# Performance work log

Hardware: AMD Instinct MI355X
Metric: run time of the kernel (lower is better)

## Reference

```python
import jax, jax.numpy as jnp
import numpy as np
import math

D_MODEL = 1024
NUM_HEADS = 16
HEAD_DIM = D_MODEL // NUM_HEADS
REPETITIONS = 3
NEG = -10000.0


def setup_inputs() -> dict:
    key = jax.random.key(0)
    ks = jax.random.split(key, 5)
    B, S = 2, 2048
    x = jax.random.normal(ks[0], (B, S, D_MODEL), dtype=jnp.float32)
    Wqkv_w = jax.random.normal(ks[1], (3 * D_MODEL, D_MODEL), dtype=jnp.float32) * (1.0 / math.sqrt(D_MODEL))
    Wqkv_b = jax.random.normal(ks[2], (3 * D_MODEL,), dtype=jnp.float32) * 0.02
    out_w = jax.random.normal(ks[3], (D_MODEL, D_MODEL), dtype=jnp.float32) * (1.0 / math.sqrt(D_MODEL))
    out_b = jax.random.normal(ks[4], (D_MODEL,), dtype=jnp.float32) * 0.02
    return {"x": x, "Wqkv_w": Wqkv_w, "Wqkv_b": Wqkv_b, "out_w": out_w, "out_b": out_b}


def _self_attention(q, k, v, mask):
    # q,k,v: (B,S,H,D); mask: (S,S) additive causal (-10000 above diagonal)
    scale = 1.0 / math.sqrt(q.shape[-1])
    scores = jnp.einsum('bthd,bshd->bhts', q, k * scale) + mask  # (B,H,S,S)
    attn = jax.nn.softmax(scores, axis=-1)
    return jnp.einsum('bhts,bshd->bthd', attn, v)  # (B,S,H,D)


def reference(x, Wqkv_w, Wqkv_b, out_w, out_b):
    B, S, _ = x.shape
    qkv = x @ Wqkv_w.T + Wqkv_b                       # (B,S,3*D_MODEL)
    qkv = qkv.reshape(B, S, 3, NUM_HEADS, HEAD_DIM)
    q, k, v = qkv[:, :, 0], qkv[:, :, 1], qkv[:, :, 2]
    mask = jnp.triu(jnp.full((S, S), NEG, dtype=x.dtype), 1)
    context = _self_attention(q, k, v, mask)
    # recurrent re-attention: rep_dim == 'q' -> query replaced by previous context
    for _ in range(REPETITIONS - 1):
        context = _self_attention(context, k, v, mask)
    out = context.reshape(B, S, D_MODEL) @ out_w.T + out_b
    return out
```

## Files before the change

### kernel.cpp

```cpp
#include <hip/hip_runtime.h>


#define D_MODEL 1024
#define NHEADS  16
#define HD      64
#define SEQ     2048
#define BATCH   2
#define NROWS   (BATCH*SEQ)
#define NQKV    (3*D_MODEL)
#define SCL2F   0.1803368801111601f
#define MASK2   (-14426.950408889634f)

typedef __bf16 bf16x8 __attribute__((ext_vector_type(8)));
typedef float  f32x4  __attribute__((ext_vector_type(4)));
typedef unsigned short us8 __attribute__((ext_vector_type(8)));
typedef unsigned short us4 __attribute__((ext_vector_type(4)));
typedef short  s16x4  __attribute__((ext_vector_type(4)));

__device__ __forceinline__ unsigned short f2bf(float f) {
  unsigned int u = __float_as_uint(f);
  u = (u + 0x7fffu + ((u >> 16) & 1u)) >> 16;
  return (unsigned short)u;
}

union Pack8 { us8 v; unsigned short e[8]; };
union Pack4 { us4 v; unsigned short e[4]; };

__device__ __forceinline__ us8 cvt8(const float4 &a, const float4 &b) {
  Pack8 p;
  p.e[0]=f2bf(a.x); p.e[1]=f2bf(a.y); p.e[2]=f2bf(a.z); p.e[3]=f2bf(a.w);
  p.e[4]=f2bf(b.x); p.e[5]=f2bf(b.y); p.e[6]=f2bf(b.z); p.e[7]=f2bf(b.w);
  return p.v;
}

__device__ __forceinline__ void gl_lds16(const unsigned short* g, unsigned short* l) {
  __builtin_amdgcn_global_load_lds(
      (const __attribute__((address_space(1))) unsigned int*)g,
      (__attribute__((address_space(3))) unsigned int*)l, 16, 0, 0);
}

#define CVT_N1 (NROWS*D_MODEL)
#define CVT_N2 (NQKV*D_MODEL)
#define CVT_N3 (D_MODEL*D_MODEL)

__global__ __launch_bounds__(256) void cvt_all(
    const float* __restrict__ x, const float* __restrict__ wq,
    const float* __restrict__ ow,
    unsigned short* __restrict__ xb, unsigned short* __restrict__ wqb,
    unsigned short* __restrict__ owb)
{
  size_t i = ((size_t)blockIdx.x * 256 + threadIdx.x) * 8;
  const float* src; unsigned short* dst; size_t off;
  if (i < CVT_N1)                { src = x;  dst = xb;  off = i; }
  else if (i < CVT_N1 + CVT_N2)  { src = wq; dst = wqb; off = i - CVT_N1; }
  else                           { src = ow; dst = owb; off = i - CVT_N1 - CVT_N2; }
  float4 a = *(const float4*)(src + off);
  float4 b = *(const float4*)(src + off + 4);
  *(us8*)(dst + off) = cvt8(a, b);
}

__global__ __launch_bounds__(256) void qkv_gemm(
    const unsigned short* __restrict__ xb, const unsigned short* __restrict__ wqb,
    const float* __restrict__ bias,
    unsigned short* __restrict__ q, unsigned short* __restrict__ k,
    unsigned short* __restrict__ vT)
{
  __shared__ __align__(16) unsigned short As[128*64];
  __shared__ __align__(16) unsigned short Bs[128*64];
  const int tid = threadIdx.x;
  const int m0 = blockIdx.y * 128, n0 = blockIdx.x * 128;
  const int wave = tid >> 6, lane = tid & 63;
  const int wm = (wave >> 1) * 64, wn = (wave & 1) * 64;
  const int lrow = lane & 15, quad = lane >> 4;

  const int dr = lane >> 3;
  const int pg = lane & 7;
  const int sg = (pg ^ dr) * 8;
  const unsigned short* gA[4]; const unsigned short* gB[4];
  unsigned short *lA[4], *lB[4];
  #pragma unroll
  for (int i = 0; i < 4; i++) {
    int c = wave*4 + i;
    gA[i] = xb  + (size_t)(m0 + c*8 + dr) * D_MODEL + sg;
    gB[i] = wqb + (size_t)(n0 + c*8 + dr) * D_MODEL + sg;
    lA[i] = &As[c*512];
    lB[i] = &Bs[c*512];
  }
  const int px0 = (quad ^ (lrow & 7)) * 8;
  const int px1 = ((quad + 4) ^ (lrow & 7)) * 8;

  f32x4 acc[4][4];
  #pragma unroll
  for (int i = 0; i < 4; i++)
    #pragma unroll
    for (int j = 0; j < 4; j++) acc[i][j] = (f32x4){0.f,0.f,0.f,0.f};

  for (int k0 = 0; k0 < D_MODEL; k0 += 64) {
    __syncthreads();
    #pragma unroll
    for (int i = 0; i < 4; i++) { gl_lds16(gA[i] + k0, lA[i]); gl_lds16(gB[i] + k0, lB[i]); }
    __syncthreads();
    bf16x8 af[4][2], bfr[4][2];
    #pragma unroll
    for (int mf = 0; mf < 4; mf++) {
      int row = wm + mf*16 + lrow;
      af[mf][0] = *(const bf16x8*)&As[row*64 + px0];
      af[mf][1] = *(const bf16x8*)&As[row*64 + px1];
    }
    #pragma unroll
    for (int nb = 0; nb < 4; nb++) {
      int row = wn + nb*16 + lrow;
      bfr[nb][0] = *(const bf16x8*)&Bs[row*64 + px0];
      bfr[nb][1] = *(const bf16x8*)&Bs[row*64 + px1];
    }
    #pragma unroll
    for (int h = 0; h < 2; h++)
      #pragma unroll
      for (int mf = 0; mf < 4; mf++)
        #pragma unroll
        for (int nb = 0; nb < 4; nb++)
          acc[mf][nb] = __builtin_amdgcn_mfma_f32_16x16x32_bf16(af[mf][h], bfr[nb][h], acc[mf][nb], 0, 0, 0);
  }

  #pragma unroll
  for (int mf = 0; mf < 4; mf++) {
    #pragma unroll
    for (int nb = 0; nb < 4; nb++) {
      int n = n0 + wn + nb*16 + lrow;
      int which = n >> 10;
      int h  = (n >> 6) & 15;
      int hd = n & 63;
      int mb = m0 + wm + mf*16 + quad*4;
      int b  = mb >> 11;
      int s  = mb & 2047;
      float bi = bias[n];
      if (which == 2) {
        Pack4 p4;
        #pragma unroll
        for (int r = 0; r < 4; r++) p4.e[r] = f2bf(acc[mf][nb][r] + bi);
        *(us4*)&vT[((size_t)((b*NHEADS + h)*HD + hd))*SEQ + s] = p4.v;
      } else {
        unsigned short* dst = (which == 0) ? q : k;
        float scl = (which == 0) ? SCL2F : 1.0f;
        #pragma unroll
        for (int r = 0; r < 4; r++)
          dst[(size_t)((b*NHEADS + h)*SEQ + s + r)*HD + hd] = f2bf((acc[mf][nb][r] + bi) * scl);
      }
    }
  }
}

#define LDQ 72

__global__ __launch_bounds__(512, 4) void attn3(
    const unsigned short* __restrict__ qg,
    const unsigned short* __restrict__ kg,
    const unsigned short* __restrict__ vTg,
    unsigned short* __restrict__ ctx)
{
  __shared__ __align__(16) unsigned short Ks[4][64*LDQ];
  __shared__ __align__(16) unsigned short Vs[4][64*LDQ];
  unsigned short* QC = &Vs[0][0];

  const int tid  = threadIdx.x;
  const int w    = tid >> 6, lane = tid & 63;
  const int lrow = lane & 15, quad = lane >> 4;
  const int bh = blockIdx.x;
  const int yy = blockIdx.y;
  const int base = (blockIdx.x + yy) & 7;
  const int qt = (yy < 8) ? base : (15 - base);
  const unsigned short* qbase = qg  + (size_t)bh * SEQ * HD;
  const unsigned short* kbase = kg  + (size_t)bh * SEQ * HD;
  const unsigned short* vbase = vTg + (size_t)bh * HD * SEQ;
  unsigned short* cbase = ctx + (size_t)bh * SEQ * HD;

  const int srow = tid >> 3;
  const int sco  = (tid & 7) * 8;
  const int qrow = tid >> 2, qc0 = (tid & 3) * 16;
  const bool vsw = (w & 1);
  const int vq = (quad*4) ^ ((lrow >> 3) << 2);

  {
    const unsigned short* src = qbase + (size_t)(qt*128 + qrow)*HD + qc0;
    *(uint4*)&QC[qrow*LDQ + qc0]     = *(const uint4*)src;
    *(uint4*)&QC[qrow*LDQ + qc0 + 8] = *(const uint4*)(src + 8);
  }
  __syncthreads();

  bf16x8 qb0 = *(const bf16x8*)&QC[(w*16 + lrow)*LDQ + quad*8];
  bf16x8 qb1 = *(const bf16x8*)&QC[(w*16 + lrow)*LDQ + 32 + quad*8];
  __syncthreads();

  const int qwbase = qt*128 + w*16;
  const int npair = qt + 1;

  for (int rep = 0; rep < 3; ++rep) {
    f32x4 od[4];
    #pragma unroll
    for (int df = 0; df < 4; df++) od[df] = (f32x4){0.f,0.f,0.f,0.f};
    float ls = 0.f;

    uint4 ka, kb, va, vb;
    {
      const unsigned short* ks = kbase + (size_t)srow*HD + sco;
      ka = *(const uint4*)ks;  kb = *(const uint4*)(ks + 64*HD);
      const unsigned short* vs = vbase + (size_t)srow*SEQ + sco;
      va = *(const uint4*)vs;  vb = *(const uint4*)(vs + 64);
    }

    for (int t = 0; t < npair; ++t) {
      const int pb = (t & 1) * 2;
      *(uint4*)&Ks[pb][srow*LDQ + sco]   = ka;
      *(uint4*)&Ks[pb+1][srow*LDQ + sco] = kb;
      {
        uint4 vaS = vsw ? make_uint4(va.z, va.w, va.x, va.y) : va;
        uint4 vbS = vsw ? make_uint4(vb.z, vb.w, vb.x, vb.y) : vb;
        *(uint4*)&Vs[pb][srow*LDQ + sco]   = vaS;
        *(uint4*)&Vs[pb+1][srow*LDQ + sco] = vbS;
      }
      if (t + 1 < npair) {
        const unsigned short* ks = kbase + (size_t)((2*t+2)*64 + srow)*HD + sco;
        ka = *(const uint4*)ks;  kb = *(const uint4*)(ks + 64*HD);
        const unsigned short* vs = vbase + (size_t)srow*SEQ + (2*t+2)*64 + sco;
        va = *(const uint4*)vs;  vb = *(const uint4*)(vs + 64);
      }
      __syncthreads();

      #pragma unroll
      for (int half = 0; half < 2; ++half) {
        const int bb = pb + half;
        const int sbase = (2*t + half) * 64;
        if (sbase > qwbase + 15) continue;
        f32x4 sc[4];
        __builtin_amdgcn_s_setprio(1);
        #pragma unroll
        for (int sf = 0; sf < 4; sf++) {
          bf16x8 a0 = *(const bf16x8*)&Ks[bb][(sf*16 + lrow)*LDQ + quad*8];
          bf16x8 a1 = *(const bf16x8*)&Ks[bb][(sf*16 + lrow)*LDQ + 32 + quad*8];
          f32x4 z = (f32x4){0.f,0.f,0.f,0.f};
          z = __builtin_amdgcn_mfma_f32_16x16x32_bf16(a0, qb0, z, 0, 0, 0);
          z = __builtin_amdgcn_mfma_f32_16x16x32_bf16(a1, qb1, z, 0, 0, 0);
          sc[sf] = z;
        }
        __builtin_amdgcn_s_setprio(0);
        if (sbase + 63 > qwbase) {
          int ql = qwbase + lrow;
          #pragma unroll
          for (int sf = 0; sf < 4; sf++)
            #pragma unroll
            for (int r = 0; r < 4; r++)
              if (sbase + sf*16 + quad*4 + r > ql) sc[sf][r] += MASK2;
        }
        s16x4 pf[4];
        float lp = 0.f;
        #pragma unroll
        for (int sf = 0; sf < 4; sf++) {
          Pack4 pk;
          #pragma unroll
          for (int r = 0; r < 4; r++) {
            float pe = __builtin_amdgcn_exp2f(sc[sf][r]);
            lp += pe;
            pk.e[r] = __builtin_bit_cast(unsigned short, (__bf16)pe);
          }
          pf[sf] = __builtin_bit_cast(s16x4, pk.v);
        }
        ls += lp;
        __builtin_amdgcn_s_setprio(1);
        #pragma unroll
        for (int df = 0; df < 4; df++) {
          s16x4 v0 = *(const s16x4*)&Vs[bb][(df*16 + lrow)*LDQ +  0 + vq];
          s16x4 v1 = *(const s16x4*)&Vs[bb][(df*16 + lrow)*LDQ + 16 + vq];
          s16x4 v2 = *(const s16x4*)&Vs[bb][(df*16 + lrow)*LDQ + 32 + vq];
          s16x4 v3 = *(const s16x4*)&Vs[bb][(df*16 + lrow)*LDQ + 48 + vq];
          od[df] = __builtin_amdgcn_mfma_f32_16x16x16bf16_1k(v0, pf[0], od[df], 0, 0, 0);
          od[df] = __builtin_amdgcn_mfma_f32_16x16x16bf16_1k(v1, pf[1], od[df], 0, 0, 0);
          od[df] = __builtin_amdgcn_mfma_f32_16x16x16bf16_1k(v2, pf[2], od[df], 0, 0, 0);
          od[df] = __builtin_amdgcn_mfma_f32_16x16x16bf16_1k(v3, pf[3], od[df], 0, 0, 0);
        }
        __builtin_amdgcn_s_setprio(0);
      }
    }

    ls += __shfl_xor(ls, 16);
    ls += __shfl_xor(ls, 32);

    __syncthreads();
    {
      float f = ((rep < 2) ? SCL2F : 1.0f) / ls;
      #pragma unroll
      for (int df = 0; df < 4; df++) {
        Pack4 pk;
        #pragma unroll
        for (int r = 0; r < 4; r++)
          pk.e[r] = __builtin_bit_cast(unsigned short, (__bf16)(od[df][r] * f));
        *(us4*)&QC[(w*16 + lrow)*LDQ + df*16 + quad*4] = pk.v;
      }
    }
    __syncthreads();
    if (rep < 2) {
      qb0 = *(const bf16x8*)&QC[(w*16 + lrow)*LDQ + quad*8];
      qb1 = *(const bf16x8*)&QC[(w*16 + lrow)*LDQ + 32 + quad*8];
      __syncthreads();
    }
  }

  {
    unsigned short* dst = cbase + (size_t)(qt*128 + qrow)*HD + qc0;
    *(uint4*)dst       = *(const uint4*)&QC[qrow*LDQ + qc0];
    *(uint4*)(dst + 8) = *(const uint4*)&QC[qrow*LDQ + qc0 + 8];
  }
}

__global__ __launch_bounds__(256) void out_gemm(
    const unsigned short* __restrict__ ctx, const unsigned short* __restrict__ owb,
    const float* __restrict__ bias, float* __restrict__ out)
{
  __shared__ __align__(16) unsigned short As[128*64];
  __shared__ __align__(16) unsigned short Bs[64*64];
  const int tid = threadIdx.x;
  const int m0 = blockIdx.y * 128, n0 = blockIdx.x * 64;
  const int wave = tid >> 6, lane = tid & 63;
  const int wm = (wave >> 1) * 64, wn = (wave & 1) * 32;
  const int lrow = lane & 15, quad = lane >> 4;

  const int dr = lane >> 3, pg = lane & 7;
  const int sg = (pg ^ dr) * 8;
  size_t aoff[4]; unsigned short* lA[4];
  #pragma unroll
  for (int i = 0; i < 4; i++) {
    int c = wave*4 + i;
    int row = m0 + c*8 + dr;
    aoff[i] = ((size_t)((row >> 11)*NHEADS)*SEQ + (row & 2047))*HD + sg;
    lA[i] = &As[c*512];
  }
  const unsigned short* gB[2]; unsigned short* lB[2];
  #pragma unroll
  for (int j = 0; j < 2; j++) {
    int c = wave*2 + j;
    gB[j] = owb + (size_t)(n0 + c*8 + dr) * D_MODEL + sg;
    lB[j] = &Bs[c*512];
  }
  const int px0 = (quad ^ (lrow & 7)) * 8;
  const int px1 = ((quad + 4) ^ (lrow & 7)) * 8;

  f32x4 acc[4][2];
  #pragma unroll
  for (int i = 0; i < 4; i++)
    #pragma unroll
    for (int j = 0; j < 2; j++) acc[i][j] = (f32x4){0.f,0.f,0.f,0.f};

  for (int k0 = 0; k0 < D_MODEL; k0 += 64) {
    size_t hoff = (size_t)(k0 >> 6) * SEQ * HD;
    __syncthreads();
    #pragma unroll
    for (int i = 0; i < 4; i++) gl_lds16(ctx + aoff[i] + hoff, lA[i]);
    #pragma unroll
    for (int j = 0; j < 2; j++) gl_lds16(gB[j] + k0, lB[j]);
    __syncthreads();
    bf16x8 af[4][2], bfr[2][2];
    #pragma unroll
    for (int mf = 0; mf < 4; mf++) {
      int row = wm + mf*16 + lrow;
      af[mf][0] = *(const bf16x8*)&As[row*64 + px0];
      af[mf][1] = *(const bf16x8*)&As[row*64 + px1];
    }
    #pragma unroll
    for (int nb = 0; nb < 2; nb++) {
      int row = wn + nb*16 + lrow;
      bfr[nb][0] = *(const bf16x8*)&Bs[row*64 + px0];
      bfr[nb][1] = *(const bf16x8*)&Bs[row*64 + px1];
    }
    #pragma unroll
    for (int h = 0; h < 2; h++)
      #pragma unroll
      for (int mf = 0; mf < 4; mf++)
        #pragma unroll
        for (int nb = 0; nb < 2; nb++)
          acc[mf][nb] = __builtin_amdgcn_mfma_f32_16x16x32_bf16(af[mf][h], bfr[nb][h], acc[mf][nb], 0, 0, 0);
  }

  #pragma unroll
  for (int mf = 0; mf < 4; mf++) {
    #pragma unroll
    for (int nb = 0; nb < 2; nb++) {
      #pragma unroll
      for (int r = 0; r < 4; r++) {
        int mm = m0 + wm + mf*16 + quad*4 + r;
        int n  = n0 + wn + nb*16 + lrow;
        out[(size_t)mm * D_MODEL + n] = acc[mf][nb][r] + bias[n];
      }
    }
  }
}

extern "C" void kernel_launch(void* const* d_in, const int* in_sizes, int n_in,
                              void* d_out, int out_size, void* d_ws, size_t ws_size,
                              hipStream_t stream) {
  (void)in_sizes; (void)n_in; (void)out_size; (void)ws_size;
  const float* x      = (const float*)d_in[0];
  const float* Wqkv_w = (const float*)d_in[1];
  const float* Wqkv_b = (const float*)d_in[2];
  const float* out_w  = (const float*)d_in[3];
  const float* out_b  = (const float*)d_in[4];
  float* out = (float*)d_out;

  unsigned short* ws = (unsigned short*)d_ws;
  unsigned short* xb  = ws;
  unsigned short* wqb = ws + CVT_N1;
  unsigned short* owb = ws + CVT_N1 + CVT_N2;
  unsigned short* q   = ws + CVT_N1 + CVT_N2 + CVT_N3;
  unsigned short* k   = q + (size_t)NROWS*D_MODEL;
  unsigned short* vT  = k + (size_t)NROWS*D_MODEL;
  unsigned short* ctx = xb;

  cvt_all<<<(CVT_N1+CVT_N2+CVT_N3)/(256*8), 256, 0, stream>>>(x, Wqkv_w, out_w, xb, wqb, owb);
  qkv_gemm<<<dim3(NQKV/128, NROWS/128), 256, 0, stream>>>(xb, wqb, Wqkv_b, q, k, vT);
  attn3<<<dim3(BATCH*NHEADS, SEQ/128), 512, 0, stream>>>(q, k, vT, ctx);
  out_gemm<<<dim3(D_MODEL/64, NROWS/128), 256, 0, stream>>>(ctx, owb, out_b, out);
}
```

Measured before the change: 219.8 us.

## Rewrite QKV GEMM with 256x256 tiles, double-buffered LDS pipeline and staged epilogue

The QKV projection GEMM moves to 256x256 output tiles with 512 threads and double-buffered LDS. Global-to-LDS loads for the next k-tile are interleaved with MFMA phases, using vmcnt waits and raw barriers in place of full syncthreads around each tile, and setprio around the MFMA bursts. The epilogue stages results through LDS so q/k and the transposed v are written with coalesced 16-byte stores. The larger tiles raise data reuse, but the grid drops to 12x16=192 blocks, which may underfill the GPU's compute units. Register pressure also rises with 32 accumulators per thread.

```diff
diff --git a/kernel.cpp b/kernel.cpp
--- a/kernel.cpp
+++ b/kernel.cpp
@@ -59,92 +59,178 @@
   *(us8*)(dst + off) = cvt8(a, b);
 }
 
-__global__ __launch_bounds__(256) void qkv_gemm(
+#define NKT 16
+
+#define STAGE_A(APTR, T, MH) {                                                    \
+  const unsigned short* s1_ = xb + (size_t)(m0 + (MH)*64 + s8)*D_MODEL            \
+                                 + (size_t)(T)*64 + sxA;                          \
+  gl_lds16(s1_,                       (APTR) + ((MH)*64 + s8)*64 + u8*8);         \
+  gl_lds16(s1_ + (size_t)128*D_MODEL, (APTR) + (128 + (MH)*64 + s8)*64 + u8*8); }
+
+#define STAGE_B(BPTR, T, NH) {                                                    \
+  const unsigned short* s1_ = wqb + (size_t)(n0 + segB*64 + (NH)*32 + rB)*D_MODEL \
+                                  + (size_t)(T)*64 + sxB;                         \
+  gl_lds16(s1_,                       (BPTR) + (segB*64 + (NH)*32 + rB)*64 + u8*8); \
+  gl_lds16(s1_ + (size_t)128*D_MODEL, (BPTR) + ((2+segB)*64 + (NH)*32 + rB)*64 + u8*8); }
+
+#define PHQ(APTR, BPTR, MH, NH) {                                                 \
+  bf16x8 af_[4][2]; bf16x8 bf_[2][2];                                             \
+  _Pragma("unroll")                                                               \
+  for (int mf_ = 0; mf_ < 4; mf_++) {                                             \
+    int row_ = wm2*128 + ((MH)*4+mf_)*16 + lrow;                                  \
+    af_[mf_][0] = *(const bf16x8*)&(APTR)[row_*64 + ((quad  ) ^ (lrow&7))*8];     \
+    af_[mf_][1] = *(const bf16x8*)&(APTR)[row_*64 + ((quad+4) ^ (lrow&7))*8];     \
+  }                                                                               \
+  _Pragma("unroll")                                                               \
+  for (int nf_ = 0; nf_ < 2; nf_++) {                                             \
+    int row_ = wn4*64 + ((NH)*2+nf_)*16 + lrow;                                   \
+    bf_[nf_][0] = *(const bf16x8*)&(BPTR)[row_*64 + ((quad  ) ^ (lrow&7))*8];     \
+    bf_[nf_][1] = *(const bf16x8*)&(BPTR)[row_*64 + ((quad+4) ^ (lrow&7))*8];     \
+  }                                                                               \
+  __builtin_amdgcn_s_setprio(1);                                                  \
+  _Pragma("unroll")                                                               \
+  for (int kh_ = 0; kh_ < 2; kh_++)                                               \
+    _Pragma("unroll")                                                             \
+    for (int mf_ = 0; mf_ < 4; mf_++)                                             \
+      _Pragma("unroll")                                                           \
+      for (int nf_ = 0; nf_ < 2; nf_++)                                           \
+        acc[(MH)*4+mf_][(NH)*2+nf_] = __builtin_amdgcn_mfma_f32_16x16x32_bf16(    \
+            af_[mf_][kh_], bf_[nf_][kh_], acc[(MH)*4+mf_][(NH)*2+nf_], 0, 0, 0);  \
+  __builtin_amdgcn_s_setprio(0); }
+
+#define VMW4  asm volatile("s_waitcnt vmcnt(4)" ::: "memory")
+#define SBAR  __builtin_amdgcn_s_barrier()
+
+__global__ __launch_bounds__(512, 2) void qkv_gemm(
     const unsigned short* __restrict__ xb, const unsigned short* __restrict__ wqb,
     const float* __restrict__ bias,
     unsigned short* __restrict__ q, unsigned short* __restrict__ k,
     unsigned short* __restrict__ vT)
 {
-  __shared__ __align__(16) unsigned short As[128*64];
-  __shared__ __align__(16) unsigned short Bs[128*64];
+  __shared__ __align__(16) unsigned short As[2][256*64];
+  __shared__ __align__(16) unsigned short Bs[2][256*64];
   const int tid = threadIdx.x;
-  const int m0 = blockIdx.y * 128, n0 = blockIdx.x * 128;
+  const int m0 = blockIdx.y * 256, n0 = blockIdx.x * 256;
   const int wave = tid >> 6, lane = tid & 63;
-  const int wm = (wave >> 1) * 64, wn = (wave & 1) * 64;
+  const int wm2 = wave >> 2, wn4 = wave & 3;
   const int lrow = lane & 15, quad = lane >> 4;
 
-  const int dr = lane >> 3;
-  const int pg = lane & 7;
-  const int sg = (pg ^ dr) * 8;
-  const unsigned short* gA[4]; const unsigned short* gB[4];
-  unsigned short *lA[4], *lB[4];
+  const int s8 = tid >> 3;
+  const int u8 = tid & 7;
+  const int sxA = ((u8 ^ (s8 & 7)) * 8);
+  const int rB  = (tid & 255) >> 3;
+  const int segB = (tid >> 8) & 1;
+  const int sxB = ((u8 ^ (rB & 7)) * 8);
+
+  unsigned short* a0 = &As[0][0]; unsigned short* a1 = &As[1][0];
+  unsigned short* b0 = &Bs[0][0]; unsigned short* b1 = &Bs[1][0];
+
+  f32x4 acc[8][4];
   #pragma unroll
-  for (int i = 0; i < 4; i++) {
-    int c = wave*4 + i;
-    gA[i] = xb  + (size_t)(m0 + c*8 + dr) * D_MODEL + sg;
-    gB[i] = wqb + (size_t)(n0 + c*8 + dr) * D_MODEL + sg;
-    lA[i] = &As[c*512];
-    lB[i] = &Bs[c*512];
-  }
-  const int px0 = (quad ^ (lrow & 7)) * 8;
-  const int px1 = ((quad + 4) ^ (lrow & 7)) * 8;
-
-  f32x4 acc[4][4];
-  #pragma unroll
-  for (int i = 0; i < 4; i++)
+  for (int i = 0; i < 8; i++)
     #pragma unroll
     for (int j = 0; j < 4; j++) acc[i][j] = (f32x4){0.f,0.f,0.f,0.f};
 
-  for (int k0 = 0; k0 < D_MODEL; k0 += 64) {
-    __syncthreads();
-    #pragma unroll
-    for (int i = 0; i < 4; i++) { gl_lds16(gA[i] + k0, lA[i]); gl_lds16(gB[i] + k0, lB[i]); }
-    __syncthreads();
-    bf16x8 af[4][2], bfr[4][2];
-    #pragma unroll
-    for (int mf = 0; mf < 4; mf++) {
-      int row = wm + mf*16 + lrow;
-      af[mf][0] = *(const bf16x8*)&As[row*64 + px0];
-      af[mf][1] = *(const bf16x8*)&As[row*64 + px1];
-    }
-    #pragma unroll
-    for (int nb = 0; nb < 4; nb++) {
-      int row = wn + nb*16 + lrow;
-      bfr[nb][0] = *(const bf16x8*)&Bs[row*64 + px0];
-      bfr[nb][1] = *(const bf16x8*)&Bs[row*64 + px1];
-    }
-    #pragma unroll
-    for (int h = 0; h < 2; h++)
-      #pragma unroll
-      for (int mf = 0; mf < 4; mf++)
-        #pragma unroll
-        for (int nb = 0; nb < 4; nb++)
-          acc[mf][nb] = __builtin_amdgcn_mfma_f32_16x16x32_bf16(af[mf][h], bfr[nb][h], acc[mf][nb], 0, 0, 0);
-  }
-
-  #pragma unroll
-  for (int mf = 0; mf < 4; mf++) {
-    #pragma unroll
-    for (int nb = 0; nb < 4; nb++) {
-      int n = n0 + wn + nb*16 + lrow;
-      int which = n >> 10;
-      int h  = (n >> 6) & 15;
-      int hd = n & 63;
-      int mb = m0 + wm + mf*16 + quad*4;
-      int b  = mb >> 11;
-      int s  = mb & 2047;
-      float bi = bias[n];
-      if (which == 2) {
-        Pack4 p4;
-        #pragma unroll
-        for (int r = 0; r < 4; r++) p4.e[r] = f2bf(acc[mf][nb][r] + bi);
-        *(us4*)&vT[((size_t)((b*NHEADS + h)*HD + hd))*SEQ + s] = p4.v;
-      } else {
-        unsigned short* dst = (which == 0) ? q : k;
-        float scl = (which == 0) ? SCL2F : 1.0f;
-        #pragma unroll
-        for (int r = 0; r < 4; r++)
-          dst[(size_t)((b*NHEADS + h)*SEQ + s + r)*HD + hd] = f2bf((acc[mf][nb][r] + bi) * scl);
+  STAGE_A(a0, 0, 0); STAGE_B(b0, 0, 0);
+  STAGE_A(a0, 0, 1); STAGE_B(b0, 0, 1);
+  STAGE_A(a1, 1, 0); STAGE_B(b1, 1, 0);
+  VMW4; SBAR;
+
+  for (int it = 0; it < NKT/2; ++it) {
+    const int kt = 2*it;
+    const int t1 = kt + 1;
+    const int t2 = (kt + 2 < NKT) ? kt + 2 : NKT - 1;
+    const int t3 = (kt + 3 < NKT) ? kt + 3 : NKT - 1;
+    STAGE_A(a1, t1, 1); PHQ(a0, b0, 0, 0); SBAR;
+    STAGE_B(b1, t1, 1); PHQ(a0, b0, 0, 1); SBAR;
+    STAGE_A(a0, t2, 0); PHQ(a0, b0, 1, 0); SBAR;
+    STAGE_B(b0, t2, 0); PHQ(a0, b0, 1, 1); VMW4; SBAR;
+    STAGE_A(a0, t2, 1); PHQ(a1, b1, 0, 0); SBAR;
+    STAGE_B(b0, t2, 1); PHQ(a1, b1, 0, 1); SBAR;
+    STAGE_A(a1, t3, 0); PHQ(a1, b1, 1, 0); SBAR;
+    STAGE_B(b1, t3, 0); PHQ(a1, b1, 1, 1); VMW4; SBAR;
+  }
+
+  asm volatile("s_waitcnt vmcnt(0)" ::: "memory");
+  __syncthreads();
+
+  const int which = n0 >> 10;
+  const int b  = m0 >> 11;
+  const int s0 = m0 & 2047;
+  const int h0 = (n0 & 1023) >> 6;
+  unsigned short* epi = &As[0][0];
+  const int wavep = wave & 3, msub = wave >> 2;
+
+  if (which < 2) {
+    const float scl = (which == 0) ? SCL2F : 1.0f;
+    unsigned short* dstbase = (which == 0) ? q : k;
+    #pragma unroll
+    for (int ns = 0; ns < 2; ++ns) {
+      if (ns) __syncthreads();
+      if ((wn4 >> 1) == ns) {
+        unsigned short* es = epi + wm2*16384;
+        #pragma unroll
+        for (int nfg = 0; nfg < 4; ++nfg) {
+          int nloc = (wn4 & 1)*64 + nfg*16 + lrow;
+          float bi = bias[n0 + ns*128 + nloc];
+          #pragma unroll
+          for (int mfg = 0; mfg < 8; ++mfg) {
+            int ml = mfg*16 + quad*4;
+            #pragma unroll
+            for (int r = 0; r < 4; ++r)
+              es[(ml + r)*128 + nloc] = f2bf((acc[mfg][nfg][r] + bi) * scl);
+          }
+        }
+      }
+      __syncthreads();
+      {
+        int head  = h0 + ns*2 + (wavep >> 1);
+        int shalf = wavep & 1;
+        unsigned short* hb = dstbase +
+            ((size_t)((b*NHEADS + head)*SEQ + s0 + msub*128))*HD;
+        const unsigned short* es = epi + msub*16384;
+        #pragma unroll
+        for (int i2 = 0; i2 < 8; ++i2) {
+          int off = shalf*4096 + i2*512 + lane*8;
+          int s = off >> 6, slot = off & 63;
+          *(uint4*)(hb + off) = *(const uint4*)&es[s*128 + (wavep>>1)*64 + slot];
+        }
+      }
+    }
+  } else {
+    #pragma unroll
+    for (int ns = 0; ns < 2; ++ns) {
+      if (ns) __syncthreads();
+      if ((wn4 >> 1) == ns) {
+        unsigned short* es = epi + wm2*16384;
+        #pragma unroll
+        for (int nfg = 0; nfg < 4; ++nfg) {
+          int nloc = (wn4 & 1)*64 + nfg*16 + lrow;
+          float bi = bias[n0 + ns*128 + nloc];
+          int sw = (nloc & 7) << 3;
+          #pragma unroll
+          for (int mfg = 0; mfg < 8; ++mfg) {
+            int ml = mfg*16 + quad*4;
+            Pack4 p4;
+            #pragma unroll
+            for (int r = 0; r < 4; ++r) p4.e[r] = f2bf(acc[mfg][nfg][r] + bi);
+            *(us4*)&es[nloc*128 + (ml ^ sw)] = p4.v;
+          }
+        }
+      }
+      __syncthreads();
+      {
+        const unsigned short* es = epi + msub*16384;
+        #pragma unroll
+        for (int i2 = 0; i2 < 8; ++i2) {
+          int n  = wavep*32 + i2*4 + (lane >> 4);
+          int mo = (lane & 15) * 8;
+          int sw = (n & 7) << 3;
+          unsigned short* dst = vT +
+              ((size_t)((b*NHEADS + h0 + ns*2 + (n >> 6))*HD + (n & 63)))*SEQ
+              + s0 + msub*128 + mo;
+          *(uint4*)dst = *(const uint4*)&es[n*128 + (mo ^ sw)];
+        }
       }
     }
   }
@@ -414,7 +500,7 @@
   unsigned short* ctx = xb;
 
   cvt_all<<<(CVT_N1+CVT_N2+CVT_N3)/(256*8), 256, 0, stream>>>(x, Wqkv_w, out_w, xb, wqb, owb);
-  qkv_gemm<<<dim3(NQKV/128, NROWS/128), 256, 0, stream>>>(xb, wqb, Wqkv_b, q, k, vT);
+  qkv_gemm<<<dim3(NQKV/256, NROWS/256), 512, 0, stream>>>(xb, wqb, Wqkv_b, q, k, vT);
   attn3<<<dim3(BATCH*NHEADS, SEQ/128), 512, 0, stream>>>(q, k, vT, ctx);
   out_gemm<<<dim3(D_MODEL/64, NROWS/128), 256, 0, stream>>>(ctx, owb, out_b, out);
 }
```

New measurement: 222.9 us. No clear change (+1.4%).
